# Kernel tuning notes

Hardware: AMD Instinct MI355X
Metric: run time of the kernel (lower is better)

## Reference

```python
import jax, jax.numpy as jnp
import numpy as np
import math

DIM = 2048
B = 4
L = 4096
LOCAL_WINDOW = 512
GLOBAL_STRIDE = 1024
TOTAL_SEEN = 65536


def _sparse_cache_positions(total_seen):
    # Positions kept by _build_sparse_cache: local window tail + global strided.
    local_start = max(0, total_seen - LOCAL_WINDOW)
    glob = np.arange(0, local_start, GLOBAL_STRIDE)
    loc = np.arange(local_start, total_seen)
    return np.concatenate([glob, loc]).astype(np.int64)  # sorted, 576 entries


def setup_inputs() -> dict:
    key = jax.random.key(0)
    ks = jax.random.split(key, 12)
    pos = _sparse_cache_positions(TOTAL_SEEN)
    Kc = pos.shape[0]  # 576
    inp = {
        "chunk": jax.random.normal(ks[0], (B, L, DIM), dtype=jnp.float32),
        "cached_k": jax.random.normal(ks[1], (B, Kc, DIM), dtype=jnp.float32),
        "cached_v": jax.random.normal(ks[2], (B, Kc, DIM), dtype=jnp.float32),
        "cached_positions": jnp.asarray(pos),
        "total_seen": TOTAL_SEEN,
        "Wq": jax.random.normal(ks[3], (DIM, DIM), dtype=jnp.float32) * 0.02,
        "bq": jnp.zeros((DIM,), dtype=jnp.float32),
        "Wk": jax.random.normal(ks[4], (DIM, DIM), dtype=jnp.float32) * 0.02,
        "bk": jnp.zeros((DIM,), dtype=jnp.float32),
        "Wv": jax.random.normal(ks[5], (DIM, DIM), dtype=jnp.float32) * 0.02,
        "bv": jnp.zeros((DIM,), dtype=jnp.float32),
        "Wo": jax.random.normal(ks[6], (DIM, DIM), dtype=jnp.float32) * 0.02,
        "bo": jnp.zeros((DIM,), dtype=jnp.float32),
    }
    return inp


def reference(chunk, cached_k, cached_v, cached_positions, total_seen,
              Wq, bq, Wk, bk, Wv, bv, Wo, bo):
    Bn, Ln, D = chunk.shape
    scale = 1.0 / math.sqrt(D)
    # QKV projections (nn.Linear: x @ W.T + b)
    q = chunk @ Wq.T + bq            # [B, L, D]
    new_k = chunk @ Wk.T + bk        # [B, L, D]
    new_v = chunk @ Wv.T + bv
    new_pos = jnp.arange(total_seen, total_seen + Ln)  # [L]
    full_k = jnp.concatenate([cached_k, new_k], axis=1)   # [B, Kc+L, D]
    full_v = jnp.concatenate([cached_v, new_v], axis=1)
    full_pos = jnp.concatenate([cached_positions, new_pos], axis=0)  # [Kc+L]
    # Masked dense attention (causal on absolute positions)
    scores = jnp.einsum('bqd,bkd->bqk', q, full_k) * scale  # [B, L, Kc+L]
    causal = full_pos[None, :] > new_pos[:, None]           # [L, Kc+L]
    scores = jnp.where(causal[None, :, :], -jnp.inf, scores)
    weights = jax.nn.softmax(scores, axis=-1)
    attended = jnp.einsum('bqk,bkd->bqd', weights, full_v)  # [B, L, D]
    return attended @ Wo.T + bo
```

## Files before the change

kernel.cpp:

```cpp
#include <hip/hip_runtime.h>
#include <hip/hip_bf16.h>
#include <hip/hip_fp16.h>
#include <math.h>

#define B_   4
#define L_   4096
#define D_   2048
#define KC_  576
#define KT_  4672
#define KTP_ 4736

typedef __attribute__((ext_vector_type(8))) short short8;
typedef __attribute__((ext_vector_type(4))) float floatx4;

enum { EPI_BF16 = 0, EPI_KV = 1, EPI_SCORE = 2, EPI_F32 = 3 };

__device__ static inline void gl_lds16(const void* g, void* l) {
  __builtin_amdgcn_global_load_lds((const __attribute__((address_space(1))) void*)g,
                                   (__attribute__((address_space(3))) void*)l,
                                   16, 0, 0);
}

__global__ __launch_bounds__(256) void gemm_bt(
    const ushort* __restrict__ A, int lda,
    const ushort* __restrict__ Bt, int ldb,
    void* __restrict__ out, int ldo,
    const float* __restrict__ bias,
    int K, int mode, float scale)
{
  __shared__ __align__(16) ushort As[128 * 32];
  __shared__ __align__(16) ushort Bs[128 * 32];
  const int t    = threadIdx.x;
  const int lane = t & 63;
  const int wave = t >> 6;
  const int bm = blockIdx.y * 128;
  const int bn = blockIdx.x * 128;
  const int wm = (wave & 1) * 64;
  const int wn = (wave >> 1) * 64;

  floatx4 acc[4][4];
#pragma unroll
  for (int i = 0; i < 4; i++)
#pragma unroll
    for (int j = 0; j < 4; j++) acc[i][j] = (floatx4)(0.0f);

  const int srow = t >> 2;
  const int scol = (t & 3) * 8;
  const ushort* Ag = A  + (size_t)(bm + srow) * lda + scol;
  const ushort* Bg = Bt + (size_t)(bn + srow) * ldb + scol;
  char* AsB = (char*)As + wave * 1024;
  char* BsB = (char*)Bs + wave * 1024;
  const int fr = lane & 15;
  const int fq = lane >> 4;

  for (int k0 = 0; k0 < K; k0 += 32) {
    __syncthreads();
    gl_lds16(Ag + k0,                        AsB);
    gl_lds16(Ag + (size_t)64 * lda + k0,     AsB + 4096);
    gl_lds16(Bg + k0,                        BsB);
    gl_lds16(Bg + (size_t)64 * ldb + k0,     BsB + 4096);
    __syncthreads();

    short8 af[4], bf[4];
#pragma unroll
    for (int i = 0; i < 4; i++)
      af[i] = *(const short8*)(As + (wm + i * 16 + fr) * 32 + fq * 8);
#pragma unroll
    for (int j = 0; j < 4; j++)
      bf[j] = *(const short8*)(Bs + (wn + j * 16 + fr) * 32 + fq * 8);
#pragma unroll
    for (int i = 0; i < 4; i++)
#pragma unroll
      for (int j = 0; j < 4; j++)
        acc[i][j] = __builtin_amdgcn_mfma_f32_16x16x32_bf16(af[i], bf[j], acc[i][j], 0, 0, 0);
  }

#pragma unroll
  for (int i = 0; i < 4; i++) {
#pragma unroll
    for (int j = 0; j < 4; j++) {
      const int col = bn + wn + j * 16 + fr;
#pragma unroll
      for (int r = 0; r < 4; r++) {
        const int row = bm + wm + i * 16 + fq * 4 + r;
        float v = acc[i][j][r];
        if (mode == EPI_SCORE) {
          v *= scale;
          bool masked = (col >= KT_) || (col >= KC_ && (col - KC_) > row);
          if (masked) v = -65504.0f;
          ((__half*)out)[(size_t)row * ldo + col] = __float2half(v);
        } else if (mode == EPI_F32) {
          if (bias) v += bias[col];
          ((float*)out)[(size_t)row * ldo + col] = v;
        } else if (mode == EPI_KV) {
          if (bias) v += bias[col];
          const int b = row >> 12;
          const int l = row & 4095;
          ((__hip_bfloat16*)out)[((size_t)b * KTP_ + KC_ + l) * D_ + col] = __float2bfloat16(v);
        } else {
          if (bias) v += bias[col];
          ((__hip_bfloat16*)out)[(size_t)row * ldo + col] = __float2bfloat16(v);
        }
      }
    }
  }
}

__global__ __launch_bounds__(256) void cvt_f32_bf16(const float* __restrict__ in,
                                                    __hip_bfloat16* __restrict__ out, int n) {
  int i = blockIdx.x * 256 + threadIdx.x;
  int stride = gridDim.x * 256;
  for (; i < n; i += stride) out[i] = __float2bfloat16(in[i]);
}

__global__ __launch_bounds__(256) void cvt_cached(const float* __restrict__ ck,
                                                  const float* __restrict__ cv,
                                                  ushort* __restrict__ fk,
                                                  ushort* __restrict__ fv) {
  const int n = B_ * KC_ * D_;
  int i = blockIdx.x * 256 + threadIdx.x;
  int stride = gridDim.x * 256;
  for (; i < n; i += stride) {
    int b = i / (KC_ * D_);
    int rem = i - b * (KC_ * D_);
    size_t o = (size_t)b * KTP_ * D_ + rem;
    __hip_bfloat16 k16 = __float2bfloat16(ck[i]);
    __hip_bfloat16 v16 = __float2bfloat16(cv[i]);
    fk[o] = *(ushort*)&k16;
    fv[o] = *(ushort*)&v16;
  }
}

__global__ __launch_bounds__(256) void zero_pad(ushort* __restrict__ fk, ushort* __restrict__ fv) {
  const int n = B_ * (KTP_ - KT_) * D_;
  int i = blockIdx.x * 256 + threadIdx.x;
  int stride = gridDim.x * 256;
  for (; i < n; i += stride) {
    int b = i / ((KTP_ - KT_) * D_);
    int rem = i - b * ((KTP_ - KT_) * D_);
    size_t o = (size_t)b * KTP_ * D_ + (size_t)KT_ * D_ + rem;
    fk[o] = 0;
    fv[o] = 0;
  }
}

__global__ __launch_bounds__(256) void transpose_k(const ushort* __restrict__ in,
                                                   ushort* __restrict__ out) {
  __shared__ ushort tile[32][33];
  const int bx = blockIdx.x * 32;
  const int by = blockIdx.y * 32;
  const int t = threadIdx.x;
  for (int e = t; e < 1024; e += 256) {
    int r = e >> 5, c = e & 31;
    tile[r][c] = in[(size_t)(bx + r) * D_ + by + c];
  }
  __syncthreads();
  for (int e = t; e < 1024; e += 256) {
    int r = e >> 5, c = e & 31;
    out[(size_t)(by + r) * KTP_ + bx + c] = tile[c][r];
  }
}

__global__ __launch_bounds__(256) void softmax_rows(ushort* __restrict__ Sbuf) {
  const int row = blockIdx.x;
  ushort* sr = Sbuf + (size_t)row * KTP_;
  const int t = threadIdx.x;
  float vals[19];
  float m = -1e30f;
#pragma unroll
  for (int i = 0; i < 19; i++) {
    int idx = i * 256 + t;
    float v = -1e30f;
    if (idx < KTP_) v = __half2float(((const __half*)sr)[idx]);
    vals[i] = v;
    m = fmaxf(m, v);
  }
  __shared__ float red[256];
  red[t] = m;
  __syncthreads();
  for (int s = 128; s > 0; s >>= 1) {
    if (t < s) red[t] = fmaxf(red[t], red[t + s]);
    __syncthreads();
  }
  m = red[0];
  __syncthreads();
  float sum = 0.0f;
#pragma unroll
  for (int i = 0; i < 19; i++) {
    float e = __expf(vals[i] - m);
    vals[i] = e;
    sum += e;
  }
  red[t] = sum;
  __syncthreads();
  for (int s = 128; s > 0; s >>= 1) {
    if (t < s) red[t] += red[t + s];
    __syncthreads();
  }
  float inv = 1.0f / red[0];
#pragma unroll
  for (int i = 0; i < 19; i++) {
    int idx = i * 256 + t;
    if (idx < KTP_) {
      __hip_bfloat16 w = __float2bfloat16(vals[i] * inv);
      sr[idx] = *(ushort*)&w;
    }
  }
}

extern "C" void kernel_launch(void* const* d_in, const int* in_sizes, int n_in,
                              void* d_out, int out_size, void* d_ws, size_t ws_size,
                              hipStream_t stream) {
  const float* chunk    = (const float*)d_in[0];
  const float* cached_k = (const float*)d_in[1];
  const float* cached_v = (const float*)d_in[2];
  const float* Wq = (const float*)d_in[5];
  const float* bq = (const float*)d_in[6];
  const float* Wk = (const float*)d_in[7];
  const float* bk = (const float*)d_in[8];
  const float* Wv = (const float*)d_in[9];
  const float* bv = (const float*)d_in[10];
  const float* Wo = (const float*)d_in[11];
  const float* bo = (const float*)d_in[12];
  float* out = (float*)d_out;

  char* ws = (char*)d_ws;
  size_t off = 0;
  auto alloc = [&](size_t bytes) -> char* {
    char* p = ws + off;
    off += (bytes + 255) & ~(size_t)255;
    return p;
  };
  ushort* wqb = (ushort*)alloc((size_t)D_ * D_ * 2);
  ushort* wkb = (ushort*)alloc((size_t)D_ * D_ * 2);
  ushort* wvb = (ushort*)alloc((size_t)D_ * D_ * 2);
  ushort* wob = (ushort*)alloc((size_t)D_ * D_ * 2);
  ushort* cbf = (ushort*)alloc((size_t)B_ * L_ * D_ * 2);
  ushort* qbf = (ushort*)alloc((size_t)B_ * L_ * D_ * 2);
  ushort* fk  = (ushort*)alloc((size_t)B_ * KTP_ * D_ * 2);
  ushort* fv  = (ushort*)alloc((size_t)B_ * KTP_ * D_ * 2);
  ushort* Sb  = (ushort*)alloc((size_t)L_ * KTP_ * 2);
  ushort* vt  = (ushort*)alloc((size_t)D_ * KTP_ * 2);

  dim3 blk(256);

  cvt_f32_bf16<<<8192, blk, 0, stream>>>(chunk, (__hip_bfloat16*)cbf, B_ * L_ * D_);
  cvt_f32_bf16<<<2048, blk, 0, stream>>>(Wq, (__hip_bfloat16*)wqb, D_ * D_);
  cvt_f32_bf16<<<2048, blk, 0, stream>>>(Wk, (__hip_bfloat16*)wkb, D_ * D_);
  cvt_f32_bf16<<<2048, blk, 0, stream>>>(Wv, (__hip_bfloat16*)wvb, D_ * D_);
  cvt_f32_bf16<<<2048, blk, 0, stream>>>(Wo, (__hip_bfloat16*)wob, D_ * D_);
  cvt_cached<<<2048, blk, 0, stream>>>(cached_k, cached_v, fk, fv);
  zero_pad<<<512, blk, 0, stream>>>(fk, fv);

  gemm_bt<<<dim3(D_ / 128, (B_ * L_) / 128), blk, 0, stream>>>(
      cbf, D_, wqb, D_, qbf, D_, bq, D_, EPI_BF16, 1.0f);
  gemm_bt<<<dim3(D_ / 128, (B_ * L_) / 128), blk, 0, stream>>>(
      cbf, D_, wkb, D_, fk, D_, bk, D_, EPI_KV, 1.0f);
  gemm_bt<<<dim3(D_ / 128, (B_ * L_) / 128), blk, 0, stream>>>(
      cbf, D_, wvb, D_, fv, D_, bv, D_, EPI_KV, 1.0f);

  const float scale = 1.0f / sqrtf((float)D_);

  for (int b = 0; b < B_; b++) {
    const ushort* qb  = qbf + (size_t)b * L_ * D_;
    const ushort* fkb = fk  + (size_t)b * KTP_ * D_;
    const ushort* fvb = fv  + (size_t)b * KTP_ * D_;
    ushort* ab = cbf + (size_t)b * L_ * D_;

    transpose_k<<<dim3(KTP_ / 32, D_ / 32), blk, 0, stream>>>(fvb, vt);
    gemm_bt<<<dim3(KTP_ / 128, L_ / 128), blk, 0, stream>>>(
        qb, D_, fkb, D_, Sb, KTP_, nullptr, D_, EPI_SCORE, scale);
    softmax_rows<<<L_, blk, 0, stream>>>(Sb);
    gemm_bt<<<dim3(D_ / 128, L_ / 128), blk, 0, stream>>>(
        Sb, KTP_, vt, KTP_, ab, D_, nullptr, KTP_, EPI_BF16, 1.0f);
  }

  gemm_bt<<<dim3(D_ / 128, (B_ * L_) / 128), blk, 0, stream>>>(
      cbf, D_, wob, D_, out, D_, bo, D_, EPI_F32, 1.0f);
}
```

Measured before the change: 2.388 ms.

## Skip causally masked score tiles and cap PV reduction length per row block

The score GEMM now exits early for tiles that lie entirely in the causally masked region. The PV GEMM limits its reduction length to the valid key range of each 128-row block. Softmax only reads and writes entries up to that per-block cap and writes zeros for masked positions inside it, so the reduced PV GEMM still sees correct weights. The change also adds a grouped block-index swizzle to improve L2 reuse in the projection GEMMs and merges the four weight conversions into one launch. The risk is that masked tile contents are never written, so correctness depends on the softmax cap lining up exactly with the GEMM's K cap.

```diff
diff --git a/kernel.cpp b/kernel.cpp
--- a/kernel.cpp
+++ b/kernel.cpp
@@ -14,6 +14,7 @@
 typedef __attribute__((ext_vector_type(4))) float floatx4;
 
 enum { EPI_BF16 = 0, EPI_KV = 1, EPI_SCORE = 2, EPI_F32 = 3 };
+enum { FLAG_SWZ = 1, FLAG_KCAP = 2 };
 
 __device__ static inline void gl_lds16(const void* g, void* l) {
   __builtin_amdgcn_global_load_lds((const __attribute__((address_space(1))) void*)g,
@@ -26,15 +27,32 @@
     const ushort* __restrict__ Bt, int ldb,
     void* __restrict__ out, int ldo,
     const float* __restrict__ bias,
-    int K, int mode, float scale)
+    int K, int mode, int flags, float scale)
 {
   __shared__ __align__(16) ushort As[128 * 32];
   __shared__ __align__(16) ushort Bs[128 * 32];
   const int t    = threadIdx.x;
   const int lane = t & 63;
   const int wave = t >> 6;
-  const int bm = blockIdx.y * 128;
-  const int bn = blockIdx.x * 128;
+
+  int m_idx, n_idx;
+  if (flags & FLAG_SWZ) {
+    const int bid = blockIdx.x + (gridDim.x * blockIdx.y);
+    n_idx = 2 * (bid & 7) + ((bid >> 3) & 1);
+    m_idx = bid >> 4;
+  } else {
+    n_idx = blockIdx.x;
+    m_idx = blockIdx.y;
+  }
+  const int bm = m_idx * 128;
+  const int bn = n_idx * 128;
+
+  if (mode == EPI_SCORE && bn >= KC_ + bm + 128) return;
+  if (flags & FLAG_KCAP) {
+    const int kcap = 704 + 128 * m_idx;
+    if (K > kcap) K = kcap;
+  }
+
   const int wm = (wave & 1) * 64;
   const int wn = (wave >> 1) * 64;
 
@@ -113,6 +131,22 @@
   for (; i < n; i += stride) out[i] = __float2bfloat16(in[i]);
 }
 
+__global__ __launch_bounds__(256) void cvt_weights(const float* __restrict__ wq,
+                                                   const float* __restrict__ wk,
+                                                   const float* __restrict__ wv,
+                                                   const float* __restrict__ wo,
+                                                   __hip_bfloat16* __restrict__ out) {
+  const int per = D_ * D_;
+  const int n = 4 * per;
+  int i = blockIdx.x * 256 + threadIdx.x;
+  int stride = gridDim.x * 256;
+  for (; i < n; i += stride) {
+    int w = i / per, rem = i - w * per;
+    const float* src = (w == 0) ? wq : (w == 1) ? wk : (w == 2) ? wv : wo;
+    out[i] = __float2bfloat16(src[rem]);
+  }
+}
+
 __global__ __launch_bounds__(256) void cvt_cached(const float* __restrict__ ck,
                                                   const float* __restrict__ cv,
                                                   ushort* __restrict__ fk,
@@ -163,17 +197,21 @@
 
 __global__ __launch_bounds__(256) void softmax_rows(ushort* __restrict__ Sbuf) {
   const int row = blockIdx.x;
+  const int nvalid = KC_ + row + 1;
+  const int wcap = 704 + (row & ~127);
   ushort* sr = Sbuf + (size_t)row * KTP_;
   const int t = threadIdx.x;
   float vals[19];
   float m = -1e30f;
+  int nit = (wcap - t + 255) / 256;
 #pragma unroll
   for (int i = 0; i < 19; i++) {
     int idx = i * 256 + t;
     float v = -1e30f;
-    if (idx < KTP_) v = __half2float(((const __half*)sr)[idx]);
+    if (idx < nvalid) v = __half2float(((const __half*)sr)[idx]);
     vals[i] = v;
     m = fmaxf(m, v);
+    if (i + 1 >= nit) break;
   }
   __shared__ float red[256];
   red[t] = m;
@@ -187,9 +225,13 @@
   float sum = 0.0f;
 #pragma unroll
   for (int i = 0; i < 19; i++) {
-    float e = __expf(vals[i] - m);
-    vals[i] = e;
-    sum += e;
+    int idx = i * 256 + t;
+    if (idx < wcap) {
+      float e = (idx < nvalid) ? __expf(vals[i] - m) : 0.0f;
+      vals[i] = e;
+      sum += e;
+    }
+    if (i + 1 >= nit) break;
   }
   red[t] = sum;
   __syncthreads();
@@ -201,10 +243,11 @@
 #pragma unroll
   for (int i = 0; i < 19; i++) {
     int idx = i * 256 + t;
-    if (idx < KTP_) {
+    if (idx < wcap) {
       __hip_bfloat16 w = __float2bfloat16(vals[i] * inv);
       sr[idx] = *(ushort*)&w;
     }
+    if (i + 1 >= nit) break;
   }
 }
 
@@ -231,10 +274,11 @@
     off += (bytes + 255) & ~(size_t)255;
     return p;
   };
-  ushort* wqb = (ushort*)alloc((size_t)D_ * D_ * 2);
-  ushort* wkb = (ushort*)alloc((size_t)D_ * D_ * 2);
-  ushort* wvb = (ushort*)alloc((size_t)D_ * D_ * 2);
-  ushort* wob = (ushort*)alloc((size_t)D_ * D_ * 2);
+  ushort* wall = (ushort*)alloc((size_t)4 * D_ * D_ * 2);
+  ushort* wqb = wall;
+  ushort* wkb = wall + (size_t)D_ * D_;
+  ushort* wvb = wall + (size_t)2 * D_ * D_;
+  ushort* wob = wall + (size_t)3 * D_ * D_;
   ushort* cbf = (ushort*)alloc((size_t)B_ * L_ * D_ * 2);
   ushort* qbf = (ushort*)alloc((size_t)B_ * L_ * D_ * 2);
   ushort* fk  = (ushort*)alloc((size_t)B_ * KTP_ * D_ * 2);
@@ -245,19 +289,16 @@
   dim3 blk(256);
 
   cvt_f32_bf16<<<8192, blk, 0, stream>>>(chunk, (__hip_bfloat16*)cbf, B_ * L_ * D_);
-  cvt_f32_bf16<<<2048, blk, 0, stream>>>(Wq, (__hip_bfloat16*)wqb, D_ * D_);
-  cvt_f32_bf16<<<2048, blk, 0, stream>>>(Wk, (__hip_bfloat16*)wkb, D_ * D_);
-  cvt_f32_bf16<<<2048, blk, 0, stream>>>(Wv, (__hip_bfloat16*)wvb, D_ * D_);
-  cvt_f32_bf16<<<2048, blk, 0, stream>>>(Wo, (__hip_bfloat16*)wob, D_ * D_);
+  cvt_weights<<<4096, blk, 0, stream>>>(Wq, Wk, Wv, Wo, (__hip_bfloat16*)wall);
   cvt_cached<<<2048, blk, 0, stream>>>(cached_k, cached_v, fk, fv);
   zero_pad<<<512, blk, 0, stream>>>(fk, fv);
 
   gemm_bt<<<dim3(D_ / 128, (B_ * L_) / 128), blk, 0, stream>>>(
-      cbf, D_, wqb, D_, qbf, D_, bq, D_, EPI_BF16, 1.0f);
+      cbf, D_, wqb, D_, qbf, D_, bq, D_, EPI_BF16, FLAG_SWZ, 1.0f);
   gemm_bt<<<dim3(D_ / 128, (B_ * L_) / 128), blk, 0, stream>>>(
-      cbf, D_, wkb, D_, fk, D_, bk, D_, EPI_KV, 1.0f);
+      cbf, D_, wkb, D_, fk, D_, bk, D_, EPI_KV, FLAG_SWZ, 1.0f);
   gemm_bt<<<dim3(D_ / 128, (B_ * L_) / 128), blk, 0, stream>>>(
-      cbf, D_, wvb, D_, fv, D_, bv, D_, EPI_KV, 1.0f);
+      cbf, D_, wvb, D_, fv, D_, bv, D_, EPI_KV, FLAG_SWZ, 1.0f);
 
   const float scale = 1.0f / sqrtf((float)D_);
 
@@ -269,12 +310,12 @@
 
     transpose_k<<<dim3(KTP_ / 32, D_ / 32), blk, 0, stream>>>(fvb, vt);
     gemm_bt<<<dim3(KTP_ / 128, L_ / 128), blk, 0, stream>>>(
-        qb, D_, fkb, D_, Sb, KTP_, nullptr, D_, EPI_SCORE, scale);
+        qb, D_, fkb, D_, Sb, KTP_, nullptr, D_, EPI_SCORE, 0, scale);
     softmax_rows<<<L_, blk, 0, stream>>>(Sb);
     gemm_bt<<<dim3(D_ / 128, L_ / 128), blk, 0, stream>>>(
-        Sb, KTP_, vt, KTP_, ab, D_, nullptr, KTP_, EPI_BF16, 1.0f);
+        Sb, KTP_, vt, KTP_, ab, D_, nullptr, KTP_, EPI_BF16, FLAG_SWZ | FLAG_KCAP, 1.0f);
   }
 
   gemm_bt<<<dim3(D_ / 128, (B_ * L_) / 128), blk, 0, stream>>>(
-      cbf, D_, wob, D_, out, D_, bo, D_, EPI_F32, 1.0f);
-}
+      cbf, D_, wob, D_, out, D_, bo, D_, EPI_F32, FLAG_SWZ, 1.0f);
+}
```

New measurement: 2.161 ms. 1.11x faster.
